# Optimization experiments

Measured on AMD Instinct MI355X. Metric: run time of the kernel, lower is better.

## Reference

```python
import jax, jax.numpy as jnp
import numpy as np

NEG_INF = -1e9


def setup_inputs() -> dict:
    key = jax.random.key(0)
    ks = jax.random.split(key, 6)
    B, S, D, H, Dh = 2, 2048, 1024, 16, 64
    scale = 1.0 / np.sqrt(D)
    return {
        "x": jax.random.normal(ks[0], (B, S, D), jnp.float32),
        "W_Q": jax.random.normal(ks[1], (H, D, Dh), jnp.float32) * scale,
        "b_Q": jnp.zeros((H, Dh), jnp.float32),
        "W_K": jax.random.normal(ks[2], (H, D, Dh), jnp.float32) * scale,
        "b_K": jnp.zeros((H, Dh), jnp.float32),
        "W_V": jax.random.normal(ks[3], (H, D, Dh), jnp.float32) * scale,
        "W_O": jax.random.normal(ks[4], (H, Dh, D), jnp.float32) * scale,
        "b_V": jnp.zeros((H, Dh), jnp.float32),
        "b_O": jnp.zeros((H, D), jnp.float32),
    }


def reference(x, W_Q, b_Q, W_K, b_K, W_V, W_O, b_V, b_O):
    # x: [b, s, m]; W_{Q,K,V}: [h, m, d]; W_O: [h, d, m]
    S = x.shape[1]
    d_head = W_Q.shape[-1]

    q = jnp.einsum("bqm,hmd->bqhd", x, W_Q) + b_Q  # [b, q, h, d]
    k = jnp.einsum("bkm,hmd->bkhd", x, W_K) + b_K
    v = jnp.einsum("bkm,hmd->bkhd", x, W_V) + b_V

    scores = jnp.einsum("bqhd,bkhd->bhqk", q, k) / jnp.sqrt(
        jnp.asarray(d_head, x.dtype)
    )  # [b, h, q, k] -- full score matrix, as in the unfused original
    causal = jnp.tril(jnp.ones((S, S), bool))
    scores = jnp.where(causal, scores, jnp.asarray(NEG_INF, x.dtype))
    attn = jax.nn.softmax(scores, axis=-1)

    z = jnp.einsum("bhqk,bkhd->bqhd", attn, v)  # [b, q, h, d]
    # per-head output proj then sum over heads; b_O is [h, m] per the annotation
    out = jnp.einsum("bqhd,hdm->bqm", z, W_O) + jnp.sum(b_O, axis=0)
    return out
```

## Files before the change

kernel.cpp:

```cpp
#include <hip/hip_runtime.h>
#include <cstdint>

typedef unsigned short u16;
typedef short s8v __attribute__((ext_vector_type(8)));
typedef float f4v __attribute__((ext_vector_type(4)));

__device__ __forceinline__ u16 f2b(float f) {
  uint32_t u = __float_as_uint(f);
  u = (u + 0x7FFFu + ((u >> 16) & 1u)) >> 16;
  return (u16)u;
}

__device__ __forceinline__ uint32_t pk2(float a, float b) {
  uint32_t r;
  asm("v_cvt_pk_bf16_f32 %0, %1, %2" : "=v"(r) : "v"(a), "v"(b));
  return r;
}

__device__ __forceinline__ void gload16(const u16* g, u16* l) {
  __builtin_amdgcn_global_load_lds(
      (const __attribute__((address_space(1))) void*)g,
      (__attribute__((address_space(3))) void*)l, 16, 0, 0);
}

__global__ void prep(const float* __restrict__ x, u16* __restrict__ xb,
                     const float* __restrict__ WQ, const float* __restrict__ WK,
                     const float* __restrict__ WV, const float* __restrict__ WO,
                     u16* __restrict__ WTqkv, u16* __restrict__ WOT,
                     const float* __restrict__ bQ, const float* __restrict__ bK,
                     const float* __restrict__ bV, const float* __restrict__ bO,
                     float* __restrict__ bqkv, float* __restrict__ bsum) {
  __shared__ u16 tile[64][65];
  const int bid = blockIdx.x;
  const int tid = threadIdx.x;

  if (bid < 4096) {
    int i = bid * 256 + tid;
    float4 v = ((const float4*)x)[i];
    uint2 o;
    o.x = (uint32_t)f2b(v.x) | ((uint32_t)f2b(v.y) << 16);
    o.y = (uint32_t)f2b(v.z) | ((uint32_t)f2b(v.w) << 16);
    ((uint2*)xb)[i] = o;
  } else if (bid < 4864) {
    int sub = bid - 4096;
    int w = sub >> 8, sub2 = sub & 255;
    const float* W = (w == 0) ? WQ : (w == 1) ? WK : WV;
    u16* dst = WTqkv + (size_t)w * 1024 * 1024;
    const int m0 = (sub2 & 15) * 64;
    const int h  = sub2 >> 4;
    const int c  = tid & 63;
    const int r4 = tid >> 6;
    const float* Wh = W + (size_t)h * 65536;
    for (int i = 0; i < 16; ++i) {
      int lm = i * 4 + r4;
      tile[lm][c] = f2b(Wh[(size_t)(m0 + lm) * 64 + c]);
    }
    __syncthreads();
    for (int i = 0; i < 16; ++i) {
      int dd = i * 4 + r4;
      dst[((size_t)h * 64 + dd) * 1024 + m0 + c] = tile[c][dd];
    }
  } else if (bid < 5120) {
    int sub = bid - 4864;
    const int k0 = (sub & 15) * 64;
    const int m0 = (sub >> 4) * 64;
    const int c  = tid & 63;
    const int r4 = tid >> 6;
    for (int i = 0; i < 16; ++i) {
      int lk = i * 4 + r4;
      tile[lk][c] = f2b(WO[(size_t)(k0 + lk) * 1024 + m0 + c]);
    }
    __syncthreads();
    for (int i = 0; i < 16; ++i) {
      int lm = i * 4 + r4;
      WOT[(size_t)(m0 + lm) * 1024 + k0 + c] = tile[c][lm];
    }
  } else {
    int t = (bid - 5120) * 256 + tid;
    if (t < 1024)       bqkv[t] = bQ[t];
    else if (t < 2048)  bqkv[t] = bK[t - 1024];
    else if (t < 3072)  bqkv[t] = bV[t - 2048];
    else {
      int m = t - 3072;
      float s = 0.f;
      for (int hh = 0; hh < 16; ++hh) s += bO[hh * 1024 + m];
      bsum[m] = s;
    }
  }
}

template<bool OUT_F32, int BM, int BN, int NTHR, bool FUSE_VT, int BK>
__global__ void gemm_bt(const u16* __restrict__ A, const u16* __restrict__ BT,
                        const float* __restrict__ bias, void* __restrict__ Cout,
                        u16* __restrict__ VTout, int N, int K, int scale_cols) {
  constexpr int NW = NTHR / 64;
  constexpr int WM = NW / 2;
  constexpr int NJ = BN / 32;
  constexpr int NH = BK / 32;
  constexpr int ASEG = BM * 4 / NTHR;
  constexpr int BSEG = BN * 4 / NTHR;
  constexpr int STG_U16 = 2 * NH * (BM + BN) * 32;
  constexpr int CT_STRIDE = BM + 8;
  constexpr int SMEM_U16 = (FUSE_VT && BN * CT_STRIDE > STG_U16)
                               ? BN * CT_STRIDE : STG_U16;
  static_assert(BM / WM == 64, "per-wave rows must be 64");
  static_assert(BM * 4 % NTHR == 0 && BN * 4 % NTHR == 0, "staging divisibility");

  __shared__ __align__(16) u16 smem[SMEM_U16];
  u16* sA = smem;
  u16* sB = smem + 2 * NH * BM * 32;

  const int tid  = threadIdx.x;
  const int lane = tid & 63, wave = tid >> 6;
  const int wm = wave >> 1, wn = wave & 1;
  const int lq = lane & 15, quad = lane >> 4;
  const int m0 = blockIdx.y * BM, n0 = blockIdx.x * BN;

  f4v acc[4][NJ] = {};

  auto STAGE = [&](int buf, int k0) {
    for (int hh = 0; hh < NH; ++hh) {
      for (int i = 0; i < ASEG; ++i) {
        int s = tid + i * NTHR;
        int row = s >> 2, part = s & 3;
        gload16(A + (size_t)(m0 + row) * K + k0 + hh * 32 + part * 8,
                &sA[(buf * NH + hh) * BM * 32 + s * 8]);
      }
      for (int i = 0; i < BSEG; ++i) {
        int s = tid + i * NTHR;
        int row = s >> 2, part = s & 3;
        gload16(BT + (size_t)(n0 + row) * K + k0 + hh * 32 + part * 8,
                &sB[(buf * NH + hh) * BN * 32 + s * 8]);
      }
    }
  };

  STAGE(0, 0);
  __syncthreads();
  int cur = 0;
  for (int k0 = 0; k0 < K; k0 += BK) {
    if (k0 + BK < K) STAGE(cur ^ 1, k0 + BK);
    for (int hh = 0; hh < NH; ++hh) {
      s8v af[4], bfr[NJ];
      for (int i = 0; i < 4; ++i)
        af[i]  = *(const s8v*)&sA[(cur * NH + hh) * BM * 32 +
                                  (wm * 64 + i * 16 + lq) * 32 + quad * 8];
      for (int j = 0; j < NJ; ++j)
        bfr[j] = *(const s8v*)&sB[(cur * NH + hh) * BN * 32 +
                                  (wn * (BN / 2) + j * 16 + lq) * 32 + quad * 8];
      for (int i = 0; i < 4; ++i)
        for (int j = 0; j < NJ; ++j)
          acc[i][j] = __builtin_amdgcn_mfma_f32_16x16x32_bf16(af[i], bfr[j], acc[i][j], 0, 0, 0);
    }
    __syncthreads();
    cur ^= 1;
  }

  if (FUSE_VT && n0 >= 2048) {
    const int vcol0 = n0 - 2048;
    u16* ct = smem;
    for (int i = 0; i < 4; ++i)
      for (int j = 0; j < NJ; ++j) {
        int row = wm * 64 + i * 16 + quad * 4;
        int col = wn * (BN / 2) + j * 16 + lq;
        float bb = bias[n0 + col];
        uint2 w;
        w.x = pk2(acc[i][j][0] + bb, acc[i][j][1] + bb);
        w.y = pk2(acc[i][j][2] + bb, acc[i][j][3] + bb);
        *(uint2*)&ct[col * CT_STRIDE + row] = w;
      }
    __syncthreads();
    if (tid < BN * 2) {
      int cc = tid >> 1, half = tid & 1;
      const uint4* src = (const uint4*)&ct[cc * CT_STRIDE + half * (BM / 2)];
      uint4* dst = (uint4*)&VTout[(size_t)(vcol0 + cc) * 4096 + m0 + half * (BM / 2)];
#pragma unroll
      for (int k = 0; k < BM / 16; ++k) dst[k] = src[k];
    }
    return;
  }

  for (int i = 0; i < 4; ++i)
    for (int j = 0; j < NJ; ++j) {
      int row = m0 + wm * 64 + i * 16 + quad * 4;
      int col = n0 + wn * (BN / 2) + j * 16 + lq;
      float bb = bias[col];
      float sc = (col < scale_cols) ? 0.125f : 1.0f;
      for (int r = 0; r < 4; ++r) {
        float v = (acc[i][j][r] + bb) * sc;
        if (OUT_F32) ((float*)Cout)[(size_t)(row + r) * N + col] = v;
        else         ((u16*)Cout)[(size_t)(row + r) * N + col] = f2b(v);
      }
    }
}

__global__ __launch_bounds__(64, 2) void attn_fwd(const u16* __restrict__ QKV,
                                                  const u16* __restrict__ VT,
                                                  u16* __restrict__ Z) {
  __shared__ __align__(16) u16 sP[2][2][16 * 72];
  const int lane = threadIdx.x;
  const int lq = lane & 15, quad = lane >> 4;

  const int id   = blockIdx.x;
  const int xcd  = id & 7;
  const int slot = id >> 3;
  const int g    = xcd + 8 * (slot >> 6);
  const int s    = slot & 63;
  const int u    = (s < 32) ? (63 - s) : (s - 32);
  const int h = g & 15, b = g >> 4;
  const int qA = u * 32, qB = qA + 16;
  const int nchunk = u / 2 + 1;

  const int RS = 3072;
  const u16* base = QKV + (size_t)b * 2048 * RS;
  const u16* Qb  = base + h * 64;
  const u16* Kb  = base + 1024 + h * 64;
  const u16* VTb = VT + (size_t)h * 64 * 4096 + (size_t)b * 2048;

  s8v qfA0 = *(const s8v*)&Qb[(size_t)(qA + lq) * RS + quad * 8];
  s8v qfA1 = *(const s8v*)&Qb[(size_t)(qA + lq) * RS + 32 + quad * 8];
  s8v qfB0 = *(const s8v*)&Qb[(size_t)(qB + lq) * RS + quad * 8];
  s8v qfB1 = *(const s8v*)&Qb[(size_t)(qB + lq) * RS + 32 + quad * 8];

  f4v zA[4] = {}, zB[4] = {};
  float mA = -3.0e38f, lA = 0.f, mB = -3.0e38f, lB = 0.f;

  s8v kf[8], vf[8];

#define LOADK(c_) do {                                                        \
    const int kk0_ = (c_) * 64;                                               \
    _Pragma("unroll")                                                         \
    for (int i_ = 0; i_ < 4; ++i_) {                                          \
      const u16* kr_ = &Kb[(size_t)(kk0_ + 16 * i_ + lq) * RS + quad * 8];    \
      kf[2 * i_]     = *(const s8v*)kr_;                                      \
      kf[2 * i_ + 1] = *(const s8v*)(kr_ + 32);                               \
    }                                                                         \
  } while (0)

#define LOADV(c_) do {                                                        \
    const int kk0_ = (c_) * 64;                                               \
    _Pragma("unroll")                                                         \
    for (int d_ = 0; d_ < 4; ++d_) {                                          \
      const u16* vr_ = &VTb[(size_t)(d_ * 16 + lq) * 4096 + kk0_ + quad * 8]; \
      vf[d_]     = *(const s8v*)vr_;                                          \
      vf[d_ + 4] = *(const s8v*)(vr_ + 32);                                   \
    }                                                                         \
  } while (0)

  auto SMW = [&](int c, int qt0, float& mrow, float& lsum, f4v (&zacc)[4],
                 u16* sPt, f4v (&sc)[4]) {
    float sv[4][4];
    for (int i = 0; i < 4; ++i)
      for (int r = 0; r < 4; ++r) sv[i][r] = sc[i][r];
    if (c + 1 == nchunk) {
      const int kb = c * 64;
      for (int i = 0; i < 4; ++i)
        for (int r = 0; r < 4; ++r)
          if (kb + 16 * i + quad * 4 + r > qt0 + lq) sv[i][r] = -3.0e38f;
    }
    float lmax = sv[0][0];
    for (int i = 0; i < 4; ++i)
      for (int r = 0; r < 4; ++r) lmax = fmaxf(lmax, sv[i][r]);
    if (!__all(lmax <= mrow + 8.0f)) {
      float t = lmax;
      t = fmaxf(t, __shfl_xor(t, 16, 64));
      t = fmaxf(t, __shfl_xor(t, 32, 64));
      float mnew = fmaxf(mrow, t);
      float al = __expf(mrow - mnew);
      mrow = mnew;
      lsum *= al;
      float alr[4];
      for (int r = 0; r < 4; ++r) alr[r] = __shfl(al, quad * 4 + r, 16);
      for (int dc = 0; dc < 4; ++dc)
        for (int r = 0; r < 4; ++r) zacc[dc][r] *= alr[r];
    }
    float acc = 0.f;
    float p[4][4];
    for (int i = 0; i < 4; ++i)
      for (int r = 0; r < 4; ++r) {
        p[i][r] = __expf(sv[i][r] - mrow);
        acc += p[i][r];
      }
    lsum += acc;
    for (int i = 0; i < 4; ++i) {
      uint2 w;
      w.x = pk2(p[i][0], p[i][1]);
      w.y = pk2(p[i][2], p[i][3]);
      *(uint2*)&sPt[lq * 72 + 16 * i + quad * 4] = w;
    }
  };

#define QK(aA_, aB_) do {                                                     \
    _Pragma("unroll")                                                         \
    for (int i_ = 0; i_ < 4; ++i_) {                                          \
      aA_[i_] = __builtin_amdgcn_mfma_f32_16x16x32_bf16(kf[2*i_],   qfA0, aA_[i_], 0, 0, 0); \
      aA_[i_] = __builtin_amdgcn_mfma_f32_16x16x32_bf16(kf[2*i_+1], qfA1, aA_[i_], 0, 0, 0); \
      aB_[i_] = __builtin_amdgcn_mfma_f32_16x16x32_bf16(kf[2*i_],   qfB0, aB_[i_], 0, 0, 0); \
      aB_[i_] = __builtin_amdgcn_mfma_f32_16x16x32_bf16(kf[2*i_+1], qfB1, aB_[i_], 0, 0, 0); \
    }                                                                         \
  } while (0)

  auto PV = [&](int pb) {
    s8v pA0 = *(const s8v*)&sP[0][pb][lq * 72 + quad * 8];
    s8v pA1 = *(const s8v*)&sP[0][pb][lq * 72 + 32 + quad * 8];
    s8v pB0 = *(const s8v*)&sP[1][pb][lq * 72 + quad * 8];
    s8v pB1 = *(const s8v*)&sP[1][pb][lq * 72 + 32 + quad * 8];
#pragma unroll
    for (int d_ = 0; d_ < 4; ++d_) {
      zA[d_] = __builtin_amdgcn_mfma_f32_16x16x32_bf16(pA0, vf[d_],     zA[d_], 0, 0, 0);
      zA[d_] = __builtin_amdgcn_mfma_f32_16x16x32_bf16(pA1, vf[d_ + 4], zA[d_], 0, 0, 0);
      zB[d_] = __builtin_amdgcn_mfma_f32_16x16x32_bf16(pB0, vf[d_],     zB[d_], 0, 0, 0);
      zB[d_] = __builtin_amdgcn_mfma_f32_16x16x32_bf16(pB1, vf[d_ + 4], zB[d_], 0, 0, 0);
    }
  };

  LOADK(0);
  {
    f4v aA[4] = {}, aB[4] = {};
    __builtin_amdgcn_s_setprio(1);
    QK(aA, aB);
    __builtin_amdgcn_s_setprio(0);
    if (nchunk > 1) LOADK(1);
    LOADV(0);
    SMW(0, qA, mA, lA, zA, sP[0][0], aA);
    SMW(0, qB, mB, lB, zB, sP[1][0], aB);
    asm volatile("" ::: "memory");
  }

  for (int c = 1; c < nchunk; ++c) {
    f4v aA[4] = {}, aB[4] = {};
    __builtin_amdgcn_s_setprio(1);
    QK(aA, aB);
    PV((c + 1) & 1);
    __builtin_amdgcn_s_setprio(0);
    asm volatile("" ::: "memory");
    if (c + 1 < nchunk) LOADK(c + 1);
    LOADV(c);
    SMW(c, qA, mA, lA, zA, sP[0][c & 1], aA);
    SMW(c, qB, mB, lB, zB, sP[1][c & 1], aB);
    asm volatile("" ::: "memory");
  }

  {
    __builtin_amdgcn_s_setprio(1);
    PV((nchunk - 1) & 1);
    __builtin_amdgcn_s_setprio(0);
  }
#undef QK
#undef LOADK
#undef LOADV

  lA += __shfl_xor(lA, 16, 64); lA += __shfl_xor(lA, 32, 64);
  lB += __shfl_xor(lB, 16, 64); lB += __shfl_xor(lB, 32, 64);
  float invA[4], invB[4];
  for (int r = 0; r < 4; ++r) {
    invA[r] = 1.0f / __shfl(lA, quad * 4 + r, 16);
    invB[r] = 1.0f / __shfl(lB, quad * 4 + r, 16);
  }
  for (int dc = 0; dc < 4; ++dc)
    for (int r = 0; r < 4; ++r) {
      size_t rowA = (size_t)b * 2048 + qA + quad * 4 + r;
      size_t rowB = (size_t)b * 2048 + qB + quad * 4 + r;
      Z[rowA * 1024 + h * 64 + dc * 16 + lq] = f2b(zA[dc][r] * invA[r]);
      Z[rowB * 1024 + h * 64 + dc * 16 + lq] = f2b(zB[dc][r] * invB[r]);
    }
}

extern "C" void kernel_launch(void* const* d_in, const int* in_sizes, int n_in,
                              void* d_out, int out_size, void* d_ws, size_t ws_size,
                              hipStream_t stream) {
  const float* x  = (const float*)d_in[0];
  const float* WQ = (const float*)d_in[1];
  const float* bQ = (const float*)d_in[2];
  const float* WK = (const float*)d_in[3];
  const float* bK = (const float*)d_in[4];
  const float* WV = (const float*)d_in[5];
  const float* WO = (const float*)d_in[6];
  const float* bV = (const float*)d_in[7];
  const float* bO = (const float*)d_in[8];
  float* out = (float*)d_out;

  uint8_t* ws = (uint8_t*)d_ws;
  u16*   xb    = (u16*)(ws);
  u16*   WTqkv = (u16*)(ws + 8388608);
  u16*   WOT   = (u16*)(ws + 14680064);
  u16*   QKV   = (u16*)(ws + 16777216);
  u16*   Zb    = (u16*)(ws + 41943040);
  float* bqkv  = (float*)(ws + 50331648);
  float* bsum  = (float*)(ws + 50343936);
  u16*   VTv   = (u16*)(ws + 50348032);

  prep<<<5136, 256, 0, stream>>>(x, xb, WQ, WK, WV, WO, WTqkv, WOT,
                                 bQ, bK, bV, bO, bqkv, bsum);
  gemm_bt<false, 128, 128, 256, true, 32><<<dim3(24, 32), 256, 0, stream>>>(
      xb, WTqkv, bqkv, (void*)QKV, VTv, 3072, 1024, 1024);
  attn_fwd<<<dim3(2048, 1, 1), 64, 0, stream>>>(QKV, VTv, Zb);
  gemm_bt<true, 128, 64, 256, false, 64><<<dim3(16, 32), 256, 0, stream>>>(
      Zb, WOT, bsum, (void*)out, nullptr, 1024, 1024, 0);
}
```

Measured before the change: 207.9 us.

## Process 64 query rows per attention wave with 32-key chunks

```diff
diff --git a/kernel.cpp b/kernel.cpp
--- a/kernel.cpp
+++ b/kernel.cpp
@@ -197,19 +197,20 @@
 __global__ __launch_bounds__(64, 2) void attn_fwd(const u16* __restrict__ QKV,
                                                   const u16* __restrict__ VT,
                                                   u16* __restrict__ Z) {
-  __shared__ __align__(16) u16 sP[2][2][16 * 72];
+  __shared__ __align__(16) u16 sP[4][2][16 * 40];
   const int lane = threadIdx.x;
   const int lq = lane & 15, quad = lane >> 4;
 
   const int id   = blockIdx.x;
   const int xcd  = id & 7;
   const int slot = id >> 3;
-  const int g    = xcd + 8 * (slot >> 6);
-  const int s    = slot & 63;
-  const int u    = (s < 32) ? (63 - s) : (s - 32);
+  const int cwx  = slot >> 5;
+  const int s    = slot & 31;
+  const int v    = (s < 16) ? (31 - s) : (s - 16);
+  const int g    = xcd + 8 * cwx;
   const int h = g & 15, b = g >> 4;
-  const int qA = u * 32, qB = qA + 16;
-  const int nchunk = u / 2 + 1;
+  const int q0 = v * 64;
+  const int nchunk = 2 * v + 2;
 
   const int RS = 3072;
   const u16* base = QKV + (size_t)b * 2048 * RS;
@@ -217,127 +218,121 @@
   const u16* Kb  = base + 1024 + h * 64;
   const u16* VTb = VT + (size_t)h * 64 * 4096 + (size_t)b * 2048;
 
-  s8v qfA0 = *(const s8v*)&Qb[(size_t)(qA + lq) * RS + quad * 8];
-  s8v qfA1 = *(const s8v*)&Qb[(size_t)(qA + lq) * RS + 32 + quad * 8];
-  s8v qfB0 = *(const s8v*)&Qb[(size_t)(qB + lq) * RS + quad * 8];
-  s8v qfB1 = *(const s8v*)&Qb[(size_t)(qB + lq) * RS + 32 + quad * 8];
-
-  f4v zA[4] = {}, zB[4] = {};
-  float mA = -3.0e38f, lA = 0.f, mB = -3.0e38f, lB = 0.f;
-
-  s8v kf[8], vf[8];
+  s8v qf[4][2];
+#pragma unroll
+  for (int t = 0; t < 4; ++t) {
+    qf[t][0] = *(const s8v*)&Qb[(size_t)(q0 + 16 * t + lq) * RS + quad * 8];
+    qf[t][1] = *(const s8v*)&Qb[(size_t)(q0 + 16 * t + lq) * RS + 32 + quad * 8];
+  }
+
+  f4v z[4][4] = {};
+  float mrow[4], lsum[4];
+#pragma unroll
+  for (int t = 0; t < 4; ++t) { mrow[t] = -3.0e38f; lsum[t] = 0.f; }
+
+  s8v kf[4], vf[4];
 
 #define LOADK(c_) do {                                                        \
-    const int kk0_ = (c_) * 64;                                               \
+    const int kk0_ = (c_) * 32;                                               \
+    const u16* kr0_ = &Kb[(size_t)(kk0_ + lq) * RS + quad * 8];               \
+    const u16* kr1_ = &Kb[(size_t)(kk0_ + 16 + lq) * RS + quad * 8];          \
+    kf[0] = *(const s8v*)kr0_;                                                \
+    kf[1] = *(const s8v*)(kr0_ + 32);                                         \
+    kf[2] = *(const s8v*)kr1_;                                                \
+    kf[3] = *(const s8v*)(kr1_ + 32);                                         \
+  } while (0)
+
+#define LOADV(c_) do {                                                        \
+    const int kk0_ = (c_) * 32;                                               \
     _Pragma("unroll")                                                         \
-    for (int i_ = 0; i_ < 4; ++i_) {                                          \
-      const u16* kr_ = &Kb[(size_t)(kk0_ + 16 * i_ + lq) * RS + quad * 8];    \
-      kf[2 * i_]     = *(const s8v*)kr_;                                      \
-      kf[2 * i_ + 1] = *(const s8v*)(kr_ + 32);                               \
-    }                                                                         \
+    for (int d_ = 0; d_ < 4; ++d_)                                            \
+      vf[d_] = *(const s8v*)&VTb[(size_t)(d_ * 16 + lq) * 4096 + kk0_ + quad * 8]; \
   } while (0)
 
-#define LOADV(c_) do {                                                        \
-    const int kk0_ = (c_) * 64;                                               \
-    _Pragma("unroll")                                                         \
-    for (int d_ = 0; d_ < 4; ++d_) {                                          \
-      const u16* vr_ = &VTb[(size_t)(d_ * 16 + lq) * 4096 + kk0_ + quad * 8]; \
-      vf[d_]     = *(const s8v*)vr_;                                          \
-      vf[d_ + 4] = *(const s8v*)(vr_ + 32);                                   \
-    }                                                                         \
-  } while (0)
-
-  auto SMW = [&](int c, int qt0, float& mrow, float& lsum, f4v (&zacc)[4],
-                 u16* sPt, f4v (&sc)[4]) {
-    float sv[4][4];
-    for (int i = 0; i < 4; ++i)
-      for (int r = 0; r < 4; ++r) sv[i][r] = sc[i][r];
-    if (c + 1 == nchunk) {
-      const int kb = c * 64;
-      for (int i = 0; i < 4; ++i)
-        for (int r = 0; r < 4; ++r)
-          if (kb + 16 * i + quad * 4 + r > qt0 + lq) sv[i][r] = -3.0e38f;
-    }
-    float lmax = sv[0][0];
-    for (int i = 0; i < 4; ++i)
-      for (int r = 0; r < 4; ++r) lmax = fmaxf(lmax, sv[i][r]);
-    if (!__all(lmax <= mrow + 8.0f)) {
-      float t = lmax;
-      t = fmaxf(t, __shfl_xor(t, 16, 64));
-      t = fmaxf(t, __shfl_xor(t, 32, 64));
-      float mnew = fmaxf(mrow, t);
-      float al = __expf(mrow - mnew);
-      mrow = mnew;
-      lsum *= al;
+  auto SMW = [&](int c, int t, f4v sacc0, f4v sacc1) {
+    float s0[4], s1[4];
+    for (int r = 0; r < 4; ++r) { s0[r] = sacc0[r]; s1[r] = sacc1[r]; }
+    if (c >= nchunk - 2) {
+      const int kb = c * 32, qt0 = q0 + 16 * t;
+      for (int r = 0; r < 4; ++r) {
+        if (kb + quad * 4 + r > qt0 + lq)      s0[r] = -3.0e38f;
+        if (kb + 16 + quad * 4 + r > qt0 + lq) s1[r] = -3.0e38f;
+      }
+    }
+    float lmax = fmaxf(fmaxf(fmaxf(s0[0], s0[1]), fmaxf(s0[2], s0[3])),
+                       fmaxf(fmaxf(s1[0], s1[1]), fmaxf(s1[2], s1[3])));
+    if (!__all(lmax <= mrow[t] + 8.0f)) {
+      float tt = lmax;
+      tt = fmaxf(tt, __shfl_xor(tt, 16, 64));
+      tt = fmaxf(tt, __shfl_xor(tt, 32, 64));
+      float mnew = fmaxf(mrow[t], tt);
+      float al = __expf(mrow[t] - mnew);
+      mrow[t] = mnew;
+      lsum[t] *= al;
       float alr[4];
       for (int r = 0; r < 4; ++r) alr[r] = __shfl(al, quad * 4 + r, 16);
       for (int dc = 0; dc < 4; ++dc)
-        for (int r = 0; r < 4; ++r) zacc[dc][r] *= alr[r];
-    }
-    float acc = 0.f;
-    float p[4][4];
-    for (int i = 0; i < 4; ++i)
-      for (int r = 0; r < 4; ++r) {
-        p[i][r] = __expf(sv[i][r] - mrow);
-        acc += p[i][r];
-      }
-    lsum += acc;
-    for (int i = 0; i < 4; ++i) {
-      uint2 w;
-      w.x = pk2(p[i][0], p[i][1]);
-      w.y = pk2(p[i][2], p[i][3]);
-      *(uint2*)&sPt[lq * 72 + 16 * i + quad * 4] = w;
-    }
+        for (int r = 0; r < 4; ++r) z[t][dc][r] *= alr[r];
+    }
+    float p0[4], p1[4], acc = 0.f;
+    for (int r = 0; r < 4; ++r) {
+      p0[r] = __expf(s0[r] - mrow[t]);
+      p1[r] = __expf(s1[r] - mrow[t]);
+      acc += p0[r] + p1[r];
+    }
+    lsum[t] += acc;
+    uint2 wlo, whi;
+    wlo.x = pk2(p0[0], p0[1]); wlo.y = pk2(p0[2], p0[3]);
+    whi.x = pk2(p1[0], p1[1]); whi.y = pk2(p1[2], p1[3]);
+    u16* rowp = &sP[t][c & 1][lq * 40 + quad * 4];
+    *(uint2*)rowp        = wlo;
+    *(uint2*)(rowp + 16) = whi;
   };
 
-#define QK(aA_, aB_) do {                                                     \
+#define QK(a0_, a1_) do {                                                     \
     _Pragma("unroll")                                                         \
-    for (int i_ = 0; i_ < 4; ++i_) {                                          \
-      aA_[i_] = __builtin_amdgcn_mfma_f32_16x16x32_bf16(kf[2*i_],   qfA0, aA_[i_], 0, 0, 0); \
-      aA_[i_] = __builtin_amdgcn_mfma_f32_16x16x32_bf16(kf[2*i_+1], qfA1, aA_[i_], 0, 0, 0); \
-      aB_[i_] = __builtin_amdgcn_mfma_f32_16x16x32_bf16(kf[2*i_],   qfB0, aB_[i_], 0, 0, 0); \
-      aB_[i_] = __builtin_amdgcn_mfma_f32_16x16x32_bf16(kf[2*i_+1], qfB1, aB_[i_], 0, 0, 0); \
+    for (int t_ = 0; t_ < 4; ++t_) {                                          \
+      a0_[t_] = __builtin_amdgcn_mfma_f32_16x16x32_bf16(kf[0], qf[t_][0], a0_[t_], 0, 0, 0); \
+      a0_[t_] = __builtin_amdgcn_mfma_f32_16x16x32_bf16(kf[1], qf[t_][1], a0_[t_], 0, 0, 0); \
+      a1_[t_] = __builtin_amdgcn_mfma_f32_16x16x32_bf16(kf[2], qf[t_][0], a1_[t_], 0, 0, 0); \
+      a1_[t_] = __builtin_amdgcn_mfma_f32_16x16x32_bf16(kf[3], qf[t_][1], a1_[t_], 0, 0, 0); \
     }                                                                         \
   } while (0)
 
   auto PV = [&](int pb) {
-    s8v pA0 = *(const s8v*)&sP[0][pb][lq * 72 + quad * 8];
-    s8v pA1 = *(const s8v*)&sP[0][pb][lq * 72 + 32 + quad * 8];
-    s8v pB0 = *(const s8v*)&sP[1][pb][lq * 72 + quad * 8];
-    s8v pB1 = *(const s8v*)&sP[1][pb][lq * 72 + 32 + quad * 8];
-#pragma unroll
-    for (int d_ = 0; d_ < 4; ++d_) {
-      zA[d_] = __builtin_amdgcn_mfma_f32_16x16x32_bf16(pA0, vf[d_],     zA[d_], 0, 0, 0);
-      zA[d_] = __builtin_amdgcn_mfma_f32_16x16x32_bf16(pA1, vf[d_ + 4], zA[d_], 0, 0, 0);
-      zB[d_] = __builtin_amdgcn_mfma_f32_16x16x32_bf16(pB0, vf[d_],     zB[d_], 0, 0, 0);
-      zB[d_] = __builtin_amdgcn_mfma_f32_16x16x32_bf16(pB1, vf[d_ + 4], zB[d_], 0, 0, 0);
+#pragma unroll
+    for (int t = 0; t < 4; ++t) {
+      s8v pf = *(const s8v*)&sP[t][pb][lq * 40 + quad * 8];
+#pragma unroll
+      for (int dc = 0; dc < 4; ++dc)
+        z[t][dc] = __builtin_amdgcn_mfma_f32_16x16x32_bf16(pf, vf[dc], z[t][dc], 0, 0, 0);
     }
   };
 
   LOADK(0);
   {
-    f4v aA[4] = {}, aB[4] = {};
+    f4v a0[4] = {}, a1[4] = {};
     __builtin_amdgcn_s_setprio(1);
-    QK(aA, aB);
+    QK(a0, a1);
     __builtin_amdgcn_s_setprio(0);
-    if (nchunk > 1) LOADK(1);
+    LOADK(1);
     LOADV(0);
-    SMW(0, qA, mA, lA, zA, sP[0][0], aA);
-    SMW(0, qB, mB, lB, zB, sP[1][0], aB);
+#pragma unroll
+    for (int t = 0; t < 4; ++t) SMW(0, t, a0[t], a1[t]);
     asm volatile("" ::: "memory");
   }
 
   for (int c = 1; c < nchunk; ++c) {
-    f4v aA[4] = {}, aB[4] = {};
+    f4v a0[4] = {}, a1[4] = {};
     __builtin_amdgcn_s_setprio(1);
-    QK(aA, aB);
+    QK(a0, a1);
     PV((c + 1) & 1);
     __builtin_amdgcn_s_setprio(0);
     asm volatile("" ::: "memory");
     if (c + 1 < nchunk) LOADK(c + 1);
     LOADV(c);
-    SMW(c, qA, mA, lA, zA, sP[0][c & 1], aA);
-    SMW(c, qB, mB, lB, zB, sP[1][c & 1], aB);
+#pragma unroll
+    for (int t = 0; t < 4; ++t) SMW(c, t, a0[t], a1[t]);
     asm volatile("" ::: "memory");
   }
 
@@ -350,20 +345,22 @@
 #undef LOADK
 #undef LOADV
 
-  lA += __shfl_xor(lA, 16, 64); lA += __shfl_xor(lA, 32, 64);
-  lB += __shfl_xor(lB, 16, 64); lB += __shfl_xor(lB, 32, 64);
-  float invA[4], invB[4];
-  for (int r = 0; r < 4; ++r) {
-    invA[r] = 1.0f / __shfl(lA, quad * 4 + r, 16);
-    invB[r] = 1.0f / __shfl(lB, quad * 4 + r, 16);
-  }
-  for (int dc = 0; dc < 4; ++dc)
-    for (int r = 0; r < 4; ++r) {
-      size_t rowA = (size_t)b * 2048 + qA + quad * 4 + r;
-      size_t rowB = (size_t)b * 2048 + qB + quad * 4 + r;
-      Z[rowA * 1024 + h * 64 + dc * 16 + lq] = f2b(zA[dc][r] * invA[r]);
-      Z[rowB * 1024 + h * 64 + dc * 16 + lq] = f2b(zB[dc][r] * invB[r]);
-    }
+#pragma unroll
+  for (int t = 0; t < 4; ++t) {
+    lsum[t] += __shfl_xor(lsum[t], 16, 64);
+    lsum[t] += __shfl_xor(lsum[t], 32, 64);
+  }
+#pragma unroll
+  for (int t = 0; t < 4; ++t) {
+    float inv[4];
+    for (int r = 0; r < 4; ++r)
+      inv[r] = 1.0f / __shfl(lsum[t], quad * 4 + r, 16);
+    for (int dc = 0; dc < 4; ++dc)
+      for (int r = 0; r < 4; ++r) {
+        size_t row = (size_t)b * 2048 + q0 + 16 * t + quad * 4 + r;
+        Z[row * 1024 + h * 64 + dc * 16 + lq] = f2b(z[t][dc][r] * inv[r]);
+      }
+  }
 }
 
 extern "C" void kernel_launch(void* const* d_in, const int* in_sizes, int n_in,
@@ -394,7 +391,7 @@
                                  bQ, bK, bV, bO, bqkv, bsum);
   gemm_bt<false, 128, 128, 256, true, 32><<<dim3(24, 32), 256, 0, stream>>>(
       xb, WTqkv, bqkv, (void*)QKV, VTv, 3072, 1024, 1024);
-  attn_fwd<<<dim3(2048, 1, 1), 64, 0, stream>>>(QKV, VTv, Zb);
+  attn_fwd<<<dim3(1024, 1, 1), 64, 0, stream>>>(QKV, VTv, Zb);
   gemm_bt<true, 128, 64, 256, false, 64><<<dim3(16, 32), 256, 0, stream>>>(
       Zb, WOT, bsum, (void*)out, nullptr, 1024, 1024, 0);
 }
```

Result: slower. 230.2 us (+10.8%).

## Software-pipeline attention loop to overlap softmax of previous chunk with QK MFMAs

Applied to the files above, without the earlier changes.

```diff
diff --git a/kernel.cpp b/kernel.cpp
--- a/kernel.cpp
+++ b/kernel.cpp
@@ -225,7 +225,9 @@
   f4v zA[4] = {}, zB[4] = {};
   float mA = -3.0e38f, lA = 0.f, mB = -3.0e38f, lB = 0.f;
 
-  s8v kf[8], vf[8];
+  s8v kf[8];
+  s8v vfA[8], vfB[8];
+  f4v aXA[4] = {}, aXB[4] = {}, aYA[4] = {}, aYB[4] = {};
 
 #define LOADK(c_) do {                                                        \
     const int kk0_ = (c_) * 64;                                               \
@@ -237,15 +239,14 @@
     }                                                                         \
   } while (0)
 
-#define LOADV(c_) do {                                                        \
-    const int kk0_ = (c_) * 64;                                               \
-    _Pragma("unroll")                                                         \
-    for (int d_ = 0; d_ < 4; ++d_) {                                          \
-      const u16* vr_ = &VTb[(size_t)(d_ * 16 + lq) * 4096 + kk0_ + quad * 8]; \
-      vf[d_]     = *(const s8v*)vr_;                                          \
-      vf[d_ + 4] = *(const s8v*)(vr_ + 32);                                   \
-    }                                                                         \
-  } while (0)
+  auto LOADV = [&](int c_, s8v (&vv)[8]) {
+#pragma unroll
+    for (int d_ = 0; d_ < 4; ++d_) {
+      const u16* vr_ = &VTb[(size_t)(d_ * 16 + lq) * 4096 + c_ * 64 + quad * 8];
+      vv[d_]     = *(const s8v*)vr_;
+      vv[d_ + 4] = *(const s8v*)(vr_ + 32);
+    }
+  };
 
   auto SMW = [&](int c, int qt0, float& mrow, float& lsum, f4v (&zacc)[4],
                  u16* sPt, f4v (&sc)[4]) {
@@ -300,55 +301,76 @@
     }                                                                         \
   } while (0)
 
-  auto PV = [&](int pb) {
+  auto PV = [&](int pb, s8v (&vv)[8]) {
     s8v pA0 = *(const s8v*)&sP[0][pb][lq * 72 + quad * 8];
     s8v pA1 = *(const s8v*)&sP[0][pb][lq * 72 + 32 + quad * 8];
     s8v pB0 = *(const s8v*)&sP[1][pb][lq * 72 + quad * 8];
     s8v pB1 = *(const s8v*)&sP[1][pb][lq * 72 + 32 + quad * 8];
 #pragma unroll
     for (int d_ = 0; d_ < 4; ++d_) {
-      zA[d_] = __builtin_amdgcn_mfma_f32_16x16x32_bf16(pA0, vf[d_],     zA[d_], 0, 0, 0);
-      zA[d_] = __builtin_amdgcn_mfma_f32_16x16x32_bf16(pA1, vf[d_ + 4], zA[d_], 0, 0, 0);
-      zB[d_] = __builtin_amdgcn_mfma_f32_16x16x32_bf16(pB0, vf[d_],     zB[d_], 0, 0, 0);
-      zB[d_] = __builtin_amdgcn_mfma_f32_16x16x32_bf16(pB1, vf[d_ + 4], zB[d_], 0, 0, 0);
-    }
+      zA[d_] = __builtin_amdgcn_mfma_f32_16x16x32_bf16(pA0, vv[d_],     zA[d_], 0, 0, 0);
+      zA[d_] = __builtin_amdgcn_mfma_f32_16x16x32_bf16(pA1, vv[d_ + 4], zA[d_], 0, 0, 0);
+      zB[d_] = __builtin_amdgcn_mfma_f32_16x16x32_bf16(pB0, vv[d_],     zB[d_], 0, 0, 0);
+      zB[d_] = __builtin_amdgcn_mfma_f32_16x16x32_bf16(pB1, vv[d_ + 4], zB[d_], 0, 0, 0);
+    }
+  };
+
+  auto STEP = [&](int c, f4v (&cA)[4], f4v (&cB)[4],
+                  f4v (&pA)[4], f4v (&pB)[4], s8v (&vfc)[8]) {
+#pragma unroll
+    for (int i = 0; i < 4; ++i) { cA[i] = (f4v){}; cB[i] = (f4v){}; }
+    __builtin_amdgcn_s_setprio(1);
+    QK(cA, cB);
+    if (c >= 2) PV(c & 1, vfc);
+    __builtin_amdgcn_s_setprio(0);
+    if (c + 1 < nchunk) LOADK(c + 1);
+    LOADV(c, vfc);
+    SMW(c - 1, qA, mA, lA, zA, sP[0][(c - 1) & 1], pA);
+    SMW(c - 1, qB, mB, lB, zB, sP[1][(c - 1) & 1], pB);
+    asm volatile("" ::: "memory");
   };
 
   LOADK(0);
   {
-    f4v aA[4] = {}, aB[4] = {};
     __builtin_amdgcn_s_setprio(1);
-    QK(aA, aB);
+    QK(aXA, aXB);
     __builtin_amdgcn_s_setprio(0);
     if (nchunk > 1) LOADK(1);
-    LOADV(0);
-    SMW(0, qA, mA, lA, zA, sP[0][0], aA);
-    SMW(0, qB, mB, lB, zB, sP[1][0], aB);
+    LOADV(0, vfA);
+  }
+
+  int c = 1;
+  for (; c + 1 < nchunk; c += 2) {
+    STEP(c,     aYA, aYB, aXA, aXB, vfB);
+    STEP(c + 1, aXA, aXB, aYA, aYB, vfA);
+  }
+  if (c < nchunk)
+    STEP(c, aYA, aYB, aXA, aXB, vfB);
+
+  {
+    const int L = nchunk - 1;
+    if (L >= 1) {
+      __builtin_amdgcn_s_setprio(1);
+      if (L & 1) PV((L + 1) & 1, vfA);
+      else       PV((L + 1) & 1, vfB);
+      __builtin_amdgcn_s_setprio(0);
+      asm volatile("" ::: "memory");
+    }
+    if (L & 1) {
+      SMW(L, qA, mA, lA, zA, sP[0][L & 1], aYA);
+      SMW(L, qB, mB, lB, zB, sP[1][L & 1], aYB);
+    } else {
+      SMW(L, qA, mA, lA, zA, sP[0][L & 1], aXA);
+      SMW(L, qB, mB, lB, zB, sP[1][L & 1], aXB);
+    }
     asm volatile("" ::: "memory");
-  }
-
-  for (int c = 1; c < nchunk; ++c) {
-    f4v aA[4] = {}, aB[4] = {};
     __builtin_amdgcn_s_setprio(1);
-    QK(aA, aB);
-    PV((c + 1) & 1);
-    __builtin_amdgcn_s_setprio(0);
-    asm volatile("" ::: "memory");
-    if (c + 1 < nchunk) LOADK(c + 1);
-    LOADV(c);
-    SMW(c, qA, mA, lA, zA, sP[0][c & 1], aA);
-    SMW(c, qB, mB, lB, zB, sP[1][c & 1], aB);
-    asm volatile("" ::: "memory");
-  }
-
-  {
-    __builtin_amdgcn_s_setprio(1);
-    PV((nchunk - 1) & 1);
+    if (L & 1) PV(L & 1, vfB);
+    else       PV(L & 1, vfA);
     __builtin_amdgcn_s_setprio(0);
   }
 #undef QK
 #undef LOADK
-#undef LOADV
 
   lA += __shfl_xor(lA, 16, 64); lA += __shfl_xor(lA, 32, 64);
   lB += __shfl_xor(lB, 16, 64); lB += __shfl_xor(lB, 32, 64);
```

Result: slower. 238.7 us (+14.8%).
